# Kernel optimization log

Hardware: AMD Instinct MI355X
Metric: run time of the kernel (lower is better)

The kernel has to match this reference:

```python
import jax, jax.numpy as jnp
import numpy as np

SEARCH_RANGE = 4


def setup_inputs() -> dict:
    key = jax.random.key(0)
    k1, k2 = jax.random.split(key)
    B, C, H, W = 4, 64, 256, 256
    x1 = jax.random.normal(k1, (B, C, H, W), dtype=jnp.float32)
    x2 = jax.random.normal(k2, (B, C, H, W), dtype=jnp.float32)
    return {"x1": x1, "x2": x2}


def reference(x1, x2):
    r = SEARCH_RANGE
    D = (2 * r + 1) ** 2
    B, C, H, W = x1.shape
    # zero-pad x2 so out-of-range correlations contribute 0 (matches the
    # original, which leaves those cv entries at their zero init)
    x2p = jnp.pad(x2, ((0, 0), (0, 0), (r, r), (r, r)))
    chans = [None] * D
    for i in range(-r, r + 1):
        for j in range(-r, r + 1):
            # torch cv[:, (2r+1)*i + j] wraps negative indices -> mod D
            k = ((2 * r + 1) * i + j) % D
            # x2 sample at (h - i, w - j): window of padded x2
            win = jax.lax.dynamic_slice(
                x2p, (0, 0, r - i, r - j), (B, C, H, W))
            chans[k] = jnp.sum(x1 * win, axis=1)  # [B,H,W]
    cv = jnp.stack(chans, axis=1)  # [B,D,H,W]
    return jax.nn.softmax(cv, axis=1)  # alpha=1, raw_output=False
```

## Files before the change

### kernel.cpp

```cpp
#include <hip/hip_runtime.h>
#include <stddef.h>

namespace {
constexpr int Hc = 256, Wc = 256, Cc = 64, Bc = 4, Dc = 81;
constexpr int CH = Hc * Wc;
}

#define PIN() asm volatile("" ::: "memory")
#define VMW(N) asm volatile("s_waitcnt vmcnt(" #N ")" ::: "memory")

#define GLOAD_LDS16(g, l)                                                   \
    __builtin_amdgcn_global_load_lds(                                       \
        (const __attribute__((address_space(1))) void*)(g),                 \
        (__attribute__((address_space(3))) void*)(l), 16, 0, 0)

#define DPPL(x) __builtin_amdgcn_update_dpp(0, (x), 0x138, 0xf, 0xf, true)
#define DPPR(x) __builtin_amdgcn_update_dpp(0, (x), 0x130, 0xf, 0xf, true)

typedef __fp16 half2v __attribute__((ext_vector_type(2)));

static __device__ __forceinline__ int pk2(float a, float b) {
#if __has_builtin(__builtin_amdgcn_cvt_pkrtz)
    half2v h = __builtin_amdgcn_cvt_pkrtz(a, b);
#else
    half2v h; h.x = (__fp16)a; h.y = (__fp16)b;
#endif
    return __builtin_bit_cast(int, h);
}

static __device__ __forceinline__ float dot2f(int q, int w, float c) {
#if __has_builtin(__builtin_amdgcn_fdot2)
    return __builtin_amdgcn_fdot2(__builtin_bit_cast(half2v, q),
                                  __builtin_bit_cast(half2v, w), c, false);
#else
    half2v a = __builtin_bit_cast(half2v, q);
    half2v b = __builtin_bit_cast(half2v, w);
    return c + (float)a.x * (float)b.x + (float)a.y * (float)b.y;
#endif
}

#define FMP(A0, A1, X0, X1)                                                 \
    do {                                                                    \
        const int P0_ = pk2(A0.x, A1.x), P1_ = pk2(A0.y, A1.y);             \
        const int P2_ = pk2(A0.z, A1.z), P3_ = pk2(A0.w, A1.w);             \
        const int w_[12] = {DPPL(P0_), DPPL(P1_), DPPL(P2_), DPPL(P3_),     \
                            P0_,       P1_,       P2_,       P3_,           \
                            DPPR(P0_), DPPR(P1_), DPPR(P2_), DPPR(P3_)};    \
        const int q_[4] = {pk2(X0.x, X1.x), pk2(X0.y, X1.y),                \
                           pk2(X0.z, X1.z), pk2(X0.w, X1.w)};               \
        _Pragma("unroll") for (int jj = 0; jj < 9; ++jj)                    \
            _Pragma("unroll") for (int s = 0; s < 4; ++s)                   \
                acc[jj][s] = dot2f(q_[s], w_[s - jj + 8], acc[jj][s]);      \
    } while (0)

#define ISX(T, OFF)                                                         \
    do {                                                                    \
        xq##T = *(const float4*)(x2p + (size_t)(OFF) * CH);                 \
        PIN();                                                              \
    } while (0)

#define RDX1(N0, N1, RA, RB, SLAB)                                          \
    do {                                                                    \
        N0 = *(const float4*)((SLAB) + (RA) * 256 + 4 * t);                 \
        N1 = *(const float4*)((SLAB) + (RB) * 256 + 4 * t);                 \
    } while (0)

#define GROUPN(CUR, NXT)                                                    \
    do {                                                                    \
        GLOAD_LDS16(x1g + (size_t)(8 + mwi) * CH, (NXT) + wi * 256);        \
        PIN();                                                              \
        RDX1(xn0, xn1, 2, 3, CUR); VMW(3); FMP(xq0, xq1, xc0, xc1);         \
        ISX(0, 4); ISX(1, 5);                                               \
        RDX1(xc0, xc1, 4, 5, CUR); VMW(3); FMP(xq2, xq3, xn0, xn1);         \
        ISX(2, 6); ISX(3, 7);                                               \
        RDX1(xn0, xn1, 6, 7, CUR); VMW(2); FMP(xq0, xq1, xc0, xc1);         \
        ISX(0, 8); ISX(1, 9);                                               \
        VMW(2); FMP(xq2, xq3, xn0, xn1);                                    \
        ISX(2, 10); ISX(3, 11);                                             \
        PIN(); __builtin_amdgcn_s_barrier(); PIN();                         \
        RDX1(xc0, xc1, 0, 1, NXT);                                          \
        x2p += (size_t)8 * CH; x1g += (size_t)8 * CH;                       \
    } while (0)

__global__ __launch_bounds__(576)
void corr_softmax_kernel(const float* __restrict__ x1,
                         const float* __restrict__ x2,
                         float* __restrict__ out)
{
    __shared__ __align__(16) float bufA[9 * 256];
    __shared__ __align__(16) float bufB[9 * 256];

    const int tid = threadIdx.x;
    const int wi  = tid >> 6;
    const int t   = tid & 63;
    const int mwi = (wi < 8) ? wi : 7;
    const int bid = blockIdx.x;
    const int bh  = (bid & 7) * 128 + (bid >> 3);
    const int b   = bh >> 8;
    const int h   = bh & 255;

    float acc[9][4];
#pragma unroll
    for (int jj = 0; jj < 9; ++jj)
#pragma unroll
        for (int s = 0; s < 4; ++s)
            acc[jj][s] = 0.f;

    const int r  = h + 4 - wi;
    const int rr = (r < 0) ? 0 : ((r > 255) ? 255 : r);

    const float* x2p = x2 + (size_t)b * Cc * CH + (size_t)rr * Wc + 4 * t;
    const float* x1g = x1 + (size_t)b * Cc * CH + (size_t)h * Wc + 4 * t;

    float4 xq0, xq1, xq2, xq3;
    float4 xc0, xc1, xn0, xn1;

    GLOAD_LDS16(x1g + (size_t)mwi * CH, bufA + wi * 256);
    PIN();
    ISX(0, 0); ISX(1, 1); ISX(2, 2); ISX(3, 3);
    VMW(4);
    PIN(); __builtin_amdgcn_s_barrier(); PIN();
    RDX1(xc0, xc1, 0, 1, bufA);

#pragma unroll 1
    for (int g = 0; g < 3; ++g) {
        GROUPN(bufA, bufB);
        GROUPN(bufB, bufA);
    }
    GROUPN(bufA, bufB);

    RDX1(xn0, xn1, 2, 3, bufB); VMW(2); FMP(xq0, xq1, xc0, xc1);
    ISX(0, 4); ISX(1, 5);
    RDX1(xc0, xc1, 4, 5, bufB); VMW(2); FMP(xq2, xq3, xn0, xn1);
    ISX(2, 6); ISX(3, 7);
    RDX1(xn0, xn1, 6, 7, bufB); VMW(2); FMP(xq0, xq1, xc0, xc1);
    VMW(0); FMP(xq2, xq3, xn0, xn1);

    if ((unsigned)r >= (unsigned)Hc) {
#pragma unroll
        for (int jj = 0; jj < 9; ++jj)
#pragma unroll
            for (int s = 0; s < 4; ++s)
                acc[jj][s] = 0.f;
    }

    __syncthreads();
    float* red = bufA;

    float m0, m1, m2, m3;
    {
        float v0 = acc[0][0], v1 = acc[0][1], v2 = acc[0][2], v3 = acc[0][3];
#pragma unroll
        for (int jj = 1; jj < 9; ++jj) {
            v0 = fmaxf(v0, acc[jj][0]);
            v1 = fmaxf(v1, acc[jj][1]);
            v2 = fmaxf(v2, acc[jj][2]);
            v3 = fmaxf(v3, acc[jj][3]);
        }
        m0 = v0; m1 = v1; m2 = v2; m3 = v3;
    }
    *(float4*)(red + wi * 256 + 4 * t) = make_float4(m0, m1, m2, m3);
    __syncthreads();

    float M0, M1, M2, M3;
    {
        float4 q = *(const float4*)(red + 4 * t);
        M0 = q.x; M1 = q.y; M2 = q.z; M3 = q.w;
#pragma unroll
        for (int w2 = 1; w2 < 9; ++w2) {
            float4 qq = *(const float4*)(red + w2 * 256 + 4 * t);
            M0 = fmaxf(M0, qq.x); M1 = fmaxf(M1, qq.y);
            M2 = fmaxf(M2, qq.z); M3 = fmaxf(M3, qq.w);
        }
    }

    float s0 = 0.f, s1 = 0.f, s2 = 0.f, s3 = 0.f;
#pragma unroll
    for (int jj = 0; jj < 9; ++jj) {
        acc[jj][0] = __expf(acc[jj][0] - M0); s0 += acc[jj][0];
        acc[jj][1] = __expf(acc[jj][1] - M1); s1 += acc[jj][1];
        acc[jj][2] = __expf(acc[jj][2] - M2); s2 += acc[jj][2];
        acc[jj][3] = __expf(acc[jj][3] - M3); s3 += acc[jj][3];
    }
    __syncthreads();
    *(float4*)(red + wi * 256 + 4 * t) = make_float4(s0, s1, s2, s3);
    __syncthreads();

    float S0, S1, S2, S3;
    {
        float4 q = *(const float4*)(red + 4 * t);
        S0 = q.x; S1 = q.y; S2 = q.z; S3 = q.w;
#pragma unroll
        for (int w2 = 1; w2 < 9; ++w2) {
            float4 qq = *(const float4*)(red + w2 * 256 + 4 * t);
            S0 += qq.x; S1 += qq.y; S2 += qq.z; S3 += qq.w;
        }
    }
    const float i0 = 1.0f / S0, i1 = 1.0f / S1, i2 = 1.0f / S2, i3 = 1.0f / S3;

    float* outp = out + (size_t)b * Dc * CH + (size_t)h * Wc + 4 * t;
#pragma unroll
    for (int jj = 0; jj < 9; ++jj) {
        int kc = 9 * wi + jj + 41;
        if (kc >= 81) kc -= 81;
        float4 o = make_float4(acc[jj][0] * i0, acc[jj][1] * i1,
                               acc[jj][2] * i2, acc[jj][3] * i3);
        *(float4*)(outp + (size_t)kc * CH) = o;
    }
}

extern "C" void kernel_launch(void* const* d_in, const int* in_sizes, int n_in,
                              void* d_out, int out_size, void* d_ws, size_t ws_size,
                              hipStream_t stream) {
    (void)in_sizes; (void)n_in; (void)d_ws; (void)ws_size; (void)out_size;
    const float* x1 = (const float*)d_in[0];
    const float* x2 = (const float*)d_in[1];
    float* out = (float*)d_out;
    dim3 grid(Bc * Hc);
    dim3 block(576);
    hipLaunchKernelGGL(corr_softmax_kernel, grid, block, 0, stream, x1, x2, out);
}
```

Baseline: 70.53 us.

## Preload whole x1 row into LDS as packed fp16 and deepen x2 prefetch

Replaces the double-buffered per-group async global->LDS staging of x1 with an upfront cooperative load of all 64 channels of the x1 row, converted once to packed half2 and stored in a 32KB LDS buffer. This removes the per-group barriers and the redundant per-wave fp16 packing of x1. It also doubles the in-flight x2 register prefetch from 4 to 8 float4 loads. In exchange there is a serialized prologue load before compute starts, more LDS use and more registers per thread, which may lower occupancy.

```diff
diff --git a/kernel.cpp b/kernel.cpp
--- a/kernel.cpp
+++ b/kernel.cpp
@@ -8,11 +8,6 @@
 
 #define PIN() asm volatile("" ::: "memory")
 #define VMW(N) asm volatile("s_waitcnt vmcnt(" #N ")" ::: "memory")
-
-#define GLOAD_LDS16(g, l)                                                   \
-    __builtin_amdgcn_global_load_lds(                                       \
-        (const __attribute__((address_space(1))) void*)(g),                 \
-        (__attribute__((address_space(3))) void*)(l), 16, 0, 0)
 
 #define DPPL(x) __builtin_amdgcn_update_dpp(0, (x), 0x138, 0xf, 0xf, true)
 #define DPPR(x) __builtin_amdgcn_update_dpp(0, (x), 0x130, 0xf, 0xf, true)
@@ -39,15 +34,14 @@
 #endif
 }
 
-#define FMP(A0, A1, X0, X1)                                                 \
+#define FMP(A0, A1, XI)                                                     \
     do {                                                                    \
         const int P0_ = pk2(A0.x, A1.x), P1_ = pk2(A0.y, A1.y);             \
         const int P2_ = pk2(A0.z, A1.z), P3_ = pk2(A0.w, A1.w);             \
         const int w_[12] = {DPPL(P0_), DPPL(P1_), DPPL(P2_), DPPL(P3_),     \
                             P0_,       P1_,       P2_,       P3_,           \
                             DPPR(P0_), DPPR(P1_), DPPR(P2_), DPPR(P3_)};    \
-        const int q_[4] = {pk2(X0.x, X1.x), pk2(X0.y, X1.y),                \
-                           pk2(X0.z, X1.z), pk2(X0.w, X1.w)};               \
+        const int q_[4] = {XI.x, XI.y, XI.z, XI.w};                         \
         _Pragma("unroll") for (int jj = 0; jj < 9; ++jj)                    \
             _Pragma("unroll") for (int s = 0; s < 4; ++s)                   \
                 acc[jj][s] = dot2f(q_[s], w_[s - jj + 8], acc[jj][s]);      \
@@ -59,46 +53,39 @@
         PIN();                                                              \
     } while (0)
 
-#define RDX1(N0, N1, RA, RB, SLAB)                                          \
-    do {                                                                    \
-        N0 = *(const float4*)((SLAB) + (RA) * 256 + 4 * t);                 \
-        N1 = *(const float4*)((SLAB) + (RB) * 256 + 4 * t);                 \
-    } while (0)
-
-#define GROUPN(CUR, NXT)                                                    \
-    do {                                                                    \
-        GLOAD_LDS16(x1g + (size_t)(8 + mwi) * CH, (NXT) + wi * 256);        \
-        PIN();                                                              \
-        RDX1(xn0, xn1, 2, 3, CUR); VMW(3); FMP(xq0, xq1, xc0, xc1);         \
-        ISX(0, 4); ISX(1, 5);                                               \
-        RDX1(xc0, xc1, 4, 5, CUR); VMW(3); FMP(xq2, xq3, xn0, xn1);         \
-        ISX(2, 6); ISX(3, 7);                                               \
-        RDX1(xn0, xn1, 6, 7, CUR); VMW(2); FMP(xq0, xq1, xc0, xc1);         \
-        ISX(0, 8); ISX(1, 9);                                               \
-        VMW(2); FMP(xq2, xq3, xn0, xn1);                                    \
-        ISX(2, 10); ISX(3, 11);                                             \
-        PIN(); __builtin_amdgcn_s_barrier(); PIN();                         \
-        RDX1(xc0, xc1, 0, 1, NXT);                                          \
-        x2p += (size_t)8 * CH; x1g += (size_t)8 * CH;                       \
-    } while (0)
+#define RX1(X, IDX) X = *(const int4*)&xp[(IDX) * 256 + 4 * t]
 
 __global__ __launch_bounds__(576)
 void corr_softmax_kernel(const float* __restrict__ x1,
                          const float* __restrict__ x2,
                          float* __restrict__ out)
 {
-    __shared__ __align__(16) float bufA[9 * 256];
-    __shared__ __align__(16) float bufB[9 * 256];
+    __shared__ __align__(16) int xp[32 * 256];
 
     const int tid = threadIdx.x;
     const int wi  = tid >> 6;
     const int t   = tid & 63;
-    const int mwi = (wi < 8) ? wi : 7;
     const int bid = blockIdx.x;
     const int bh  = (bid & 7) * 128 + (bid >> 3);
     const int b   = bh >> 8;
     const int h   = bh & 255;
 
+    const float* x1row = x1 + (size_t)b * Cc * CH + (size_t)h * Wc;
+#pragma unroll
+    for (int kk = 0; kk < 4; ++kk) {
+        const int T = tid + 576 * kk;
+        if (T < 2048) {
+            const int e = T >> 6, p = T & 63;
+            float4 a0 = *(const float4*)(x1row + (size_t)(2 * e) * CH + 4 * p);
+            float4 a1 = *(const float4*)(x1row + (size_t)(2 * e + 1) * CH + 4 * p);
+            int4 w;
+            w.x = pk2(a0.x, a1.x); w.y = pk2(a0.y, a1.y);
+            w.z = pk2(a0.z, a1.z); w.w = pk2(a0.w, a1.w);
+            *(int4*)&xp[e * 256 + 4 * p] = w;
+        }
+    }
+    __syncthreads();
+
     float acc[9][4];
 #pragma unroll
     for (int jj = 0; jj < 9; ++jj)
@@ -110,31 +97,27 @@
     const int rr = (r < 0) ? 0 : ((r > 255) ? 255 : r);
 
     const float* x2p = x2 + (size_t)b * Cc * CH + (size_t)rr * Wc + 4 * t;
-    const float* x1g = x1 + (size_t)b * Cc * CH + (size_t)h * Wc + 4 * t;
-
-    float4 xq0, xq1, xq2, xq3;
-    float4 xc0, xc1, xn0, xn1;
-
-    GLOAD_LDS16(x1g + (size_t)mwi * CH, bufA + wi * 256);
-    PIN();
+
+    float4 xq0, xq1, xq2, xq3, xq4, xq5, xq6, xq7;
+    int4 xa, xb;
+
     ISX(0, 0); ISX(1, 1); ISX(2, 2); ISX(3, 3);
-    VMW(4);
-    PIN(); __builtin_amdgcn_s_barrier(); PIN();
-    RDX1(xc0, xc1, 0, 1, bufA);
+    ISX(4, 4); ISX(5, 5); ISX(6, 6); ISX(7, 7);
+    RX1(xa, 0);
 
 #pragma unroll 1
-    for (int g = 0; g < 3; ++g) {
-        GROUPN(bufA, bufB);
-        GROUPN(bufB, bufA);
-    }
-    GROUPN(bufA, bufB);
-
-    RDX1(xn0, xn1, 2, 3, bufB); VMW(2); FMP(xq0, xq1, xc0, xc1);
-    ISX(0, 4); ISX(1, 5);
-    RDX1(xc0, xc1, 4, 5, bufB); VMW(2); FMP(xq2, xq3, xn0, xn1);
-    ISX(2, 6); ISX(3, 7);
-    RDX1(xn0, xn1, 6, 7, bufB); VMW(2); FMP(xq0, xq1, xc0, xc1);
-    VMW(0); FMP(xq2, xq3, xn0, xn1);
+    for (int g = 0; g < 7; ++g) {
+        const int e1 = 4 * g;
+        VMW(6); RX1(xb, e1 + 1); FMP(xq0, xq1, xa); ISX(0, 8);  ISX(1, 9);
+        VMW(6); RX1(xa, e1 + 2); FMP(xq2, xq3, xb); ISX(2, 10); ISX(3, 11);
+        VMW(6); RX1(xb, e1 + 3); FMP(xq4, xq5, xa); ISX(4, 12); ISX(5, 13);
+        VMW(6); RX1(xa, e1 + 4); FMP(xq6, xq7, xb); ISX(6, 14); ISX(7, 15);
+        x2p += (size_t)8 * CH;
+    }
+    VMW(6); RX1(xb, 29); FMP(xq0, xq1, xa);
+    VMW(4); RX1(xa, 30); FMP(xq2, xq3, xb);
+    VMW(2); RX1(xb, 31); FMP(xq4, xq5, xa);
+    VMW(0); FMP(xq6, xq7, xb);
 
     if ((unsigned)r >= (unsigned)Hc) {
 #pragma unroll
@@ -145,7 +128,7 @@
     }
 
     __syncthreads();
-    float* red = bufA;
+    float* red = (float*)xp;
 
     float m0, m1, m2, m3;
     {
```

Measured after the change: 77.14 us (median of 2 runs). +9.4%, slower.
